# Optimization experiments

Measured on AMD Instinct MI355X. Metric: run time of the kernel, lower is better.

## Reference

```python
import jax, jax.numpy as jnp
from jax import lax
import numpy as np

SIGMA = 0.05  # perturbation std (module default)


def setup_inputs() -> dict:
    key = jax.random.key(0)
    k1, k2, k3 = jax.random.split(key, 3)
    return {
        "scores": jax.random.normal(k1, (8, 32, 32), dtype=jnp.float32),      # scorer output (b, h_score, w_score)
        "x_high": jax.random.normal(k2, (8, 3, 1024, 1024), dtype=jnp.float32),
        "noise": jax.random.normal(k3, (8, 500, 1024), dtype=jnp.float32),    # (b, num_samples, d)
        "k": 16,
        "patch_size": 64,
    }


def reference(scores, x_high, noise, k, patch_size):
    b, hs, ws = scores.shape
    _, c, H, W = x_high.shape
    d = hs * ws
    n = noise.shape[1]
    p = patch_size

    # --- min-max normalize scores (as in DPS.forward) ---
    s = scores.reshape(b, d)
    smin = s.min(axis=-1, keepdims=True)
    smax = s.max(axis=-1, keepdims=True)
    s = (s - smin) / (smax - smin + 1e-5)

    # --- PerturbedTopK forward: mean of one-hot top-k over noise samples ---
    perturbed = s[:, None, :] + noise * SIGMA            # (b, n, d)
    _, idx = lax.top_k(perturbed, k)                     # (b, n, k)
    idx = jnp.sort(idx, axis=-1)
    bi = jnp.arange(b)[:, None, None]
    ki = jnp.arange(k)[None, None, :]
    # scatter-count == one_hot(idx, d).mean(axis=1) without materializing (b,n,k,d)
    indicators = jnp.zeros((b, k, d), s.dtype).at[bi, ki, idx].add(1.0 / n)
    indicators = indicators.reshape(b, k, hs, ws)

    # --- pad high-res image exactly like DPS.__init__ ---
    sh, sw = H // hs, W // ws                            # scale_h, scale_w
    top = (p - sh) // 2
    left = (p - sw) // 2
    padded_h = sh * hs + p - 1
    padded_w = sw * ws + p - 1
    x_pad = jnp.pad(x_high, ((0, 0), (0, 0), (top, padded_h - top - H), (left, padded_w - left - W)))
    # only the first (hs-1)*sh + p rows/cols are ever sliced by the loop
    Eh = (hs - 1) * sh + p
    Ew = (ws - 1) * sw + p
    x_pad = x_pad[:, :, :Eh, :Ew]

    # --- weighted patch gather: sum_{i,j} ind[b,k,i,j] * x_pad[b,c, i*sh+u, j*sw+v]
    # expressed as a dilated-kernel cross-correlation, vmapped over batch.
    def per_b(xp, w):  # xp: (c, Eh, Ew), w: (k, hs, ws)
        out = lax.conv_general_dilated(
            xp[:, None],            # lhs (c, 1, Eh, Ew): channels act as batch
            w[:, None],             # rhs (k, 1, hs, ws)
            window_strides=(1, 1),
            padding="VALID",
            rhs_dilation=(sh, sw),
        )                           # (c, k, p, p)
        return out.transpose(1, 0, 2, 3)  # (k, c, p, p)

    patches = jax.vmap(per_b)(x_pad, indicators)  # (b, k, c, p, p)
    return patches
```

## Files before the change

kernel.cpp:

```cpp
#include <hip/hip_runtime.h>

constexpr int NB = 8;
constexpr int ND = 1024;
constexpr int NS = 500;
constexpr int NK = 16;
constexpr int NC = 3;
constexpr int NH = 1024;
constexpr int NW = 1024;
constexpr int NP = 64;
constexpr int PTOP = 16;
constexpr int PLEFT = 16;
constexpr float SIGMA = 0.05f;
constexpr int OUT_ELEMS = NB * NK * NC * NP * NP;

__global__ void normalize_kernel(const float* __restrict__ scores,
                                 float* __restrict__ s_norm,
                                 int* __restrict__ counts,
                                 float* __restrict__ out) {
    int blk = blockIdx.x;
    int t = threadIdx.x;

    int4 z4 = make_int4(0, 0, 0, 0);
    ((int4*)counts)[blk * 512 + t] = z4;
    ((int4*)counts)[blk * 512 + 256 + t] = z4;
    float4 f4 = make_float4(0.f, 0.f, 0.f, 0.f);
#pragma unroll
    for (int q = 0; q < 24; q++)
        ((float4*)out)[(size_t)(blk * 256 + t) + (size_t)q * 16384] = f4;

    if (blk >= NB) return;
    int b = blk;
    float v[4];
#pragma unroll
    for (int q = 0; q < 4; q++) v[q] = scores[b * ND + t + 256 * q];
    float mn = fminf(fminf(v[0], v[1]), fminf(v[2], v[3]));
    float mx = fmaxf(fmaxf(v[0], v[1]), fmaxf(v[2], v[3]));
#pragma unroll
    for (int off = 1; off < 64; off <<= 1) {
        mn = fminf(mn, __shfl_xor(mn, off));
        mx = fmaxf(mx, __shfl_xor(mx, off));
    }
    __shared__ float smn[4], smx[4];
    int wave = t >> 6, lane = t & 63;
    if (lane == 0) { smn[wave] = mn; smx[wave] = mx; }
    __syncthreads();
    mn = fminf(fminf(smn[0], smn[1]), fminf(smn[2], smn[3]));
    mx = fmaxf(fmaxf(smx[0], smx[1]), fmaxf(smx[2], smx[3]));
    float den = mx - mn + 1e-5f;
#pragma unroll
    for (int q = 0; q < 4; q++)
        s_norm[b * ND + t + 256 * q] = (v[q] - mn) / den;
}

__global__ void topk_kernel(const float* __restrict__ s_norm,
                            const float* __restrict__ noise,
                            int* __restrict__ counts) {
    int t = threadIdx.x;
    int wave = t >> 6, lane = t & 63;
    int sid = blockIdx.x * 4 + wave;
    int b = sid / NS;

    const float* sp = s_norm + b * ND;
    const float* npp = noise + (size_t)sid * ND;

    float v[16];
#pragma unroll
    for (int q = 0; q < 16; q++) {
        int j = q * 64 + lane;
        v[q] = sp[j] + npp[j] * SIGMA;
    }

    int myj = 0x7fffffff;
    for (int it = 0; it < NK; it++) {
        float bv = v[0];
        int bq = 0;
#pragma unroll
        for (int q = 1; q < 16; q++)
            if (v[q] > bv) { bv = v[q]; bq = q; }
        int bj = bq * 64 + lane;
#pragma unroll
        for (int off = 1; off < 64; off <<= 1) {
            float ov = __shfl_xor(bv, off);
            int oj = __shfl_xor(bj, off);
            if (ov > bv || (ov == bv && oj < bj)) { bv = ov; bj = oj; }
        }
        if (lane == it) myj = bj;
        int wq = bj >> 6, wl = bj & 63;
#pragma unroll
        for (int q = 0; q < 16; q++)
            v[q] = (q == wq && lane == wl) ? -1e30f : v[q];
    }

    int rank = 0;
#pragma unroll
    for (int u = 0; u < NK; u++) {
        int other = __shfl(myj, u);
        rank += (other < myj) ? 1 : 0;
    }
    if (lane < NK)
        atomicAdd(&counts[(b * NK + rank) * ND + myj], 1);
}

__global__ void union_kernel(const int* __restrict__ counts,
                             int* __restrict__ ucell,
                             float* __restrict__ uw,
                             int* __restrict__ nunion) {
    int b = blockIdx.x;
    int t = threadIdx.x;
    int lane = t & 63, wave = t >> 6;
    const int* cp = counts + b * NK * ND;

    unsigned nz = 0;
    for (int kk = 0; kk < NK; kk++) {
        int4 c4 = *(const int4*)(cp + kk * ND + t * 4);
        if (c4.x) nz |= 1;
        if (c4.y) nz |= 2;
        if (c4.z) nz |= 4;
        if (c4.w) nz |= 8;
    }
    int cnt = __popc(nz);
    int incl = cnt;
#pragma unroll
    for (int off = 1; off < 64; off <<= 1) {
        int o = __shfl_up(incl, off);
        if (lane >= off) incl += o;
    }
    int excl = incl - cnt;
    __shared__ int wtot[4];
    if (lane == 63) wtot[wave] = incl;
    __syncthreads();
    int base = 0;
    for (int w = 0; w < wave; w++) base += wtot[w];
    int pos = base + excl;

    const float invn = 1.0f / (float)NS;
    int* up = ucell + b * ND;
    float* wp = uw + (size_t)b * ND * NK;
#pragma unroll
    for (int q = 0; q < 4; q++) {
        if (nz & (1u << q)) {
            int cell = t * 4 + q;
            int i = cell >> 5, j = cell & 31;
            int ent = (i << 15) | (j << 5) |
                      ((i == 0) ? 1 : 0) | ((i == 31) ? 2 : 0) |
                      ((j == 0) ? 4 : 0) | ((j == 31) ? 8 : 0);
            up[pos] = ent;
            for (int kk = 0; kk < NK; kk++)
                wp[(size_t)pos * NK + kk] = (float)cp[kk * ND + cell] * invn;
            pos++;
        }
    }
    if (t == 0) nunion[b] = wtot[0] + wtot[1] + wtot[2] + wtot[3];
}

__global__ void gather_kernel(const int* __restrict__ ucell,
                              const float* __restrict__ uw,
                              const int* __restrict__ nunion,
                              const float* __restrict__ x_high,
                              float* __restrict__ out) {
    int blk = blockIdx.x;
    int bc = blk % 24;
    int i32 = blk / 24;
    int gg = i32 & 15;
    int chunk = i32 >> 4;
    int b = bc / 3, c = bc % 3;
    int t = threadIdx.x;
    int x = t & 63;
    int y = gg * 4 + (t >> 6);

    int U = nunion[b];
    int half = U >> 1;
    int e0 = chunk ? half : 0;
    int e1 = chunk ? U : half;

    const float* xp = x_high + (size_t)bc * (NH * NW);
    int ym = y - PTOP;
    int xm = x - PLEFT;
    int off = ym * NW + xm;
    int mask = ((ym < 0) ? 1 : 0) | ((ym >= 32) ? 2 : 0) |
               ((xm < 0) ? 4 : 0) | ((xm >= 32) ? 8 : 0);

    const int* up = ucell + b * ND;
    const float* wp = uw + (size_t)b * ND * NK;

    float acc[16];
#pragma unroll
    for (int q = 0; q < 16; q++) acc[q] = 0.f;

#pragma unroll 2
    for (int e = e0; e < e1; e++) {
        int ent = up[e];
        bool ok = (ent & mask) == 0;
        int idx = (ent & ~15) + off;
        idx = ok ? idx : 0;
        float v = xp[idx];
        v = ok ? v : 0.f;
#pragma unroll
        for (int q = 0; q < 16; q++)
            acc[q] += wp[(size_t)e * NK + q] * v;
    }

#pragma unroll
    for (int q = 0; q < 16; q++) {
        int o = ((b * NK + q) * NC + c) * (NP * NP) + y * NP + x;
        atomicAdd(&out[o], acc[q]);
    }
}

extern "C" void kernel_launch(void* const* d_in, const int* in_sizes, int n_in,
                              void* d_out, int out_size, void* d_ws, size_t ws_size,
                              hipStream_t stream) {
    const float* scores = (const float*)d_in[0];
    const float* x_high = (const float*)d_in[1];
    const float* noise  = (const float*)d_in[2];

    char* ws = (char*)d_ws;
    float* s_norm = (float*)ws;
    int* counts   = (int*)(ws + 32 * 1024);
    int* ucell    = (int*)(ws + 544 * 1024);
    float* uw     = (float*)(ws + 576 * 1024);
    int* nunion   = (int*)(ws + 1088 * 1024);

    normalize_kernel<<<64, 256, 0, stream>>>(scores, s_norm, counts, (float*)d_out);
    topk_kernel<<<NB * NS / 4, 256, 0, stream>>>(s_norm, noise, counts);
    union_kernel<<<NB, 256, 0, stream>>>(counts, ucell, uw, nunion);
    gather_kernel<<<24 * 32, 256, 0, stream>>>(ucell, uw, nunion, x_high,
                                               (float*)d_out);
}
```

Baseline: 62.40 us.

## Split gather by k-halves, stage union weights in LDS, drop output zeroing and atomics

```diff
diff --git a/kernel.cpp b/kernel.cpp
--- a/kernel.cpp
+++ b/kernel.cpp
@@ -11,22 +11,16 @@
 constexpr int PTOP = 16;
 constexpr int PLEFT = 16;
 constexpr float SIGMA = 0.05f;
-constexpr int OUT_ELEMS = NB * NK * NC * NP * NP;
 
 __global__ void normalize_kernel(const float* __restrict__ scores,
                                  float* __restrict__ s_norm,
-                                 int* __restrict__ counts,
-                                 float* __restrict__ out) {
+                                 int* __restrict__ counts) {
     int blk = blockIdx.x;
     int t = threadIdx.x;
 
     int4 z4 = make_int4(0, 0, 0, 0);
     ((int4*)counts)[blk * 512 + t] = z4;
     ((int4*)counts)[blk * 512 + 256 + t] = z4;
-    float4 f4 = make_float4(0.f, 0.f, 0.f, 0.f);
-#pragma unroll
-    for (int q = 0; q < 24; q++)
-        ((float4*)out)[(size_t)(blk * 256 + t) + (size_t)q * 16384] = f4;
 
     if (blk >= NB) return;
     int b = blk;
@@ -153,6 +147,7 @@
     if (t == 0) nunion[b] = wtot[0] + wtot[1] + wtot[2] + wtot[3];
 }
 
+constexpr int EC = 16;
 __global__ void gather_kernel(const int* __restrict__ ucell,
                               const float* __restrict__ uw,
                               const int* __restrict__ nunion,
@@ -160,18 +155,28 @@
                               float* __restrict__ out) {
     int blk = blockIdx.x;
     int bc = blk % 24;
-    int i32 = blk / 24;
-    int gg = i32 & 15;
-    int chunk = i32 >> 4;
+    int ii = blk / 24;
+    int gg = ii & 15;
+    int kq = ii >> 4;
     int b = bc / 3, c = bc % 3;
     int t = threadIdx.x;
     int x = t & 63;
     int y = gg * 4 + (t >> 6);
 
-    int U = nunion[b];
-    int half = U >> 1;
-    int e0 = chunk ? half : 0;
-    int e1 = chunk ? U : half;
+    int m = nunion[b];
+
+    __shared__ int lc[ND];
+    __shared__ float lw[ND][8];
+
+    for (int i = t; i < m; i += 256) {
+        lc[i] = ucell[b * ND + i];
+        const float4* wsrc =
+            (const float4*)(uw + (size_t)(b * ND + i) * NK + kq * 8);
+        float4 w0 = wsrc[0], w1 = wsrc[1];
+        *(float4*)&lw[i][0] = w0;
+        *(float4*)&lw[i][4] = w1;
+    }
+    __syncthreads();
 
     const float* xp = x_high + (size_t)bc * (NH * NW);
     int ym = y - PTOP;
@@ -180,30 +185,40 @@
     int mask = ((ym < 0) ? 1 : 0) | ((ym >= 32) ? 2 : 0) |
                ((xm < 0) ? 4 : 0) | ((xm >= 32) ? 8 : 0);
 
-    const int* up = ucell + b * ND;
-    const float* wp = uw + (size_t)b * ND * NK;
-
-    float acc[16];
-#pragma unroll
-    for (int q = 0; q < 16; q++) acc[q] = 0.f;
-
-#pragma unroll 2
-    for (int e = e0; e < e1; e++) {
-        int ent = up[e];
-        bool ok = (ent & mask) == 0;
-        int idx = (ent & ~15) + off;
-        idx = ok ? idx : 0;
-        float v = xp[idx];
-        v = ok ? v : 0.f;
-#pragma unroll
-        for (int q = 0; q < 16; q++)
-            acc[q] += wp[(size_t)e * NK + q] * v;
-    }
-
-#pragma unroll
-    for (int q = 0; q < 16; q++) {
-        int o = ((b * NK + q) * NC + c) * (NP * NP) + y * NP + x;
-        atomicAdd(&out[o], acc[q]);
+    float acc[8];
+#pragma unroll
+    for (int q = 0; q < 8; q++) acc[q] = 0.f;
+
+    for (int base = 0; base < m; base += EC) {
+        float vv[EC];
+#pragma unroll
+        for (int j = 0; j < EC; j++) {
+            int ee = base + j;
+            int ent = lc[ee < m ? ee : 0];
+            bool ok = (ee < m) && ((ent & mask) == 0);
+            int idx = ok ? ((ent & ~15) + off) : 0;
+            float v = xp[idx];
+            vv[j] = ok ? v : 0.f;
+        }
+#pragma unroll
+        for (int j = 0; j < EC; j++) {
+            int ee = base + j;
+            int es = ee < m ? ee : 0;
+            float4 wa = *(const float4*)&lw[es][0];
+            float4 wb = *(const float4*)&lw[es][4];
+            float v = vv[j];
+            acc[0] += wa.x * v; acc[1] += wa.y * v;
+            acc[2] += wa.z * v; acc[3] += wa.w * v;
+            acc[4] += wb.x * v; acc[5] += wb.y * v;
+            acc[6] += wb.z * v; acc[7] += wb.w * v;
+        }
+    }
+
+#pragma unroll
+    for (int q = 0; q < 8; q++) {
+        int kk = kq * 8 + q;
+        int o = ((b * NK + kk) * NC + c) * (NP * NP) + y * NP + x;
+        out[o] = acc[q];
     }
 }
 
@@ -221,7 +236,7 @@
     float* uw     = (float*)(ws + 576 * 1024);
     int* nunion   = (int*)(ws + 1088 * 1024);
 
-    normalize_kernel<<<64, 256, 0, stream>>>(scores, s_norm, counts, (float*)d_out);
+    normalize_kernel<<<64, 256, 0, stream>>>(scores, s_norm, counts);
     topk_kernel<<<NB * NS / 4, 256, 0, stream>>>(s_norm, noise, counts);
     union_kernel<<<NB, 256, 0, stream>>>(counts, ucell, uw, nunion);
     gather_kernel<<<24 * 32, 256, 0, stream>>>(ucell, uw, nunion, x_high,
```

After: 57.57 us. 7.7% less time.

## Restructure gather to one row per block with batched loads and direct stores

Applied to the files above, without the earlier changes.

```diff
diff --git a/kernel.cpp b/kernel.cpp
--- a/kernel.cpp
+++ b/kernel.cpp
@@ -11,22 +11,16 @@
 constexpr int PTOP = 16;
 constexpr int PLEFT = 16;
 constexpr float SIGMA = 0.05f;
-constexpr int OUT_ELEMS = NB * NK * NC * NP * NP;
 
 __global__ void normalize_kernel(const float* __restrict__ scores,
                                  float* __restrict__ s_norm,
-                                 int* __restrict__ counts,
-                                 float* __restrict__ out) {
+                                 int* __restrict__ counts) {
     int blk = blockIdx.x;
     int t = threadIdx.x;
 
     int4 z4 = make_int4(0, 0, 0, 0);
     ((int4*)counts)[blk * 512 + t] = z4;
     ((int4*)counts)[blk * 512 + 256 + t] = z4;
-    float4 f4 = make_float4(0.f, 0.f, 0.f, 0.f);
-#pragma unroll
-    for (int q = 0; q < 24; q++)
-        ((float4*)out)[(size_t)(blk * 256 + t) + (size_t)q * 16384] = f4;
 
     if (blk >= NB) return;
     int b = blk;
@@ -153,58 +147,61 @@
     if (t == 0) nunion[b] = wtot[0] + wtot[1] + wtot[2] + wtot[3];
 }
 
-__global__ void gather_kernel(const int* __restrict__ ucell,
-                              const float* __restrict__ uw,
-                              const int* __restrict__ nunion,
-                              const float* __restrict__ x_high,
-                              float* __restrict__ out) {
+__global__ void __launch_bounds__(64)
+gather_kernel(const int* __restrict__ ucell,
+              const float* __restrict__ uw,
+              const int* __restrict__ nunion,
+              const float* __restrict__ x_high,
+              float* __restrict__ out) {
     int blk = blockIdx.x;
     int bc = blk % 24;
-    int i32 = blk / 24;
-    int gg = i32 & 15;
-    int chunk = i32 >> 4;
+    int y  = blk / 24;
     int b = bc / 3, c = bc % 3;
-    int t = threadIdx.x;
-    int x = t & 63;
-    int y = gg * 4 + (t >> 6);
+    int x = threadIdx.x;
 
     int U = nunion[b];
-    int half = U >> 1;
-    int e0 = chunk ? half : 0;
-    int e1 = chunk ? U : half;
-
+    const int* up = ucell + b * ND;
+    const float* wp = uw + (size_t)b * ND * NK;
     const float* xp = x_high + (size_t)bc * (NH * NW);
+
     int ym = y - PTOP;
     int xm = x - PLEFT;
     int off = ym * NW + xm;
     int mask = ((ym < 0) ? 1 : 0) | ((ym >= 32) ? 2 : 0) |
                ((xm < 0) ? 4 : 0) | ((xm >= 32) ? 8 : 0);
 
-    const int* up = ucell + b * ND;
-    const float* wp = uw + (size_t)b * ND * NK;
-
     float acc[16];
 #pragma unroll
     for (int q = 0; q < 16; q++) acc[q] = 0.f;
 
-#pragma unroll 2
-    for (int e = e0; e < e1; e++) {
-        int ent = up[e];
-        bool ok = (ent & mask) == 0;
-        int idx = (ent & ~15) + off;
-        idx = ok ? idx : 0;
-        float v = xp[idx];
-        v = ok ? v : 0.f;
-#pragma unroll
-        for (int q = 0; q < 16; q++)
-            acc[q] += wp[(size_t)e * NK + q] * v;
-    }
-
-#pragma unroll
-    for (int q = 0; q < 16; q++) {
-        int o = ((b * NK + q) * NC + c) * (NP * NP) + y * NP + x;
-        atomicAdd(&out[o], acc[q]);
-    }
+    for (int base = 0; base < U; base += 16) {
+        float vv[16];
+#pragma unroll
+        for (int j = 0; j < 16; j++) {
+            int e = base + j;
+            int ent = up[e < U ? e : 0];
+            bool ok = (e < U) && ((ent & mask) == 0);
+            int idx = ok ? ((ent & ~15) + off) : 0;
+            vv[j] = xp[idx];
+        }
+        __builtin_amdgcn_sched_barrier(0);
+#pragma unroll
+        for (int j = 0; j < 16; j++) {
+            int e = base + j;
+            int es = e < U ? e : 0;
+            int ent = up[es];
+            bool ok = (e < U) && ((ent & mask) == 0);
+            float v = ok ? vv[j] : 0.f;
+            const float* wq = wp + (size_t)es * NK;
+#pragma unroll
+            for (int q = 0; q < 16; q++)
+                acc[q] += wq[q] * v;
+        }
+    }
+
+#pragma unroll
+    for (int q = 0; q < 16; q++)
+        out[((size_t)(b * NK + q) * NC + c) * (NP * NP) + y * NP + x] = acc[q];
 }
 
 extern "C" void kernel_launch(void* const* d_in, const int* in_sizes, int n_in,
@@ -221,9 +218,9 @@
     float* uw     = (float*)(ws + 576 * 1024);
     int* nunion   = (int*)(ws + 1088 * 1024);
 
-    normalize_kernel<<<64, 256, 0, stream>>>(scores, s_norm, counts, (float*)d_out);
+    normalize_kernel<<<64, 256, 0, stream>>>(scores, s_norm, counts);
     topk_kernel<<<NB * NS / 4, 256, 0, stream>>>(s_norm, noise, counts);
     union_kernel<<<NB, 256, 0, stream>>>(counts, ucell, uw, nunion);
-    gather_kernel<<<24 * 32, 256, 0, stream>>>(ucell, uw, nunion, x_high,
-                                               (float*)d_out);
-}
+    gather_kernel<<<24 * 64, 64, 0, stream>>>(ucell, uw, nunion, x_high,
+                                              (float*)d_out);
+}
```

Measured after the change: 74.80 us. +19.9%, slower.
